# Kernel optimization log

Hardware: AMD Instinct MI355X
Metric: run time of the kernel (lower is better)

## Reference

```python
import jax, jax.numpy as jnp
import numpy as np
from jax import lax

DT = 0.01  # fixed Euler-Maruyama step size

B, N, C, M, H, T = 1024, 64, 16, 16, 512, 128


def setup_inputs() -> dict:
    key = jax.random.key(0)
    ks = jax.random.split(key, 8)
    d_in = N + C  # concat(y, control)
    inp = {
        "y0": jax.random.normal(ks[0], (B, N), jnp.float32),
        "controls": jax.random.normal(ks[1], (T, C), jnp.float32),
        "noise": jax.random.normal(ks[2], (T - 1, B, M), jnp.float32),
        # mu MLP: d_in -> H -> N
        "W1_mu": jax.random.normal(ks[3], (d_in, H), jnp.float32) / np.sqrt(d_in),
        "b1_mu": jnp.zeros((H,), jnp.float32),
        "W2_mu": jax.random.normal(ks[4], (H, N), jnp.float32) / np.sqrt(H),
        "b2_mu": jnp.zeros((N,), jnp.float32),
        # sigma MLP: d_in -> H -> N*M
        "W1_sg": jax.random.normal(ks[5], (d_in, H), jnp.float32) / np.sqrt(d_in),
        "b1_sg": jnp.zeros((H,), jnp.float32),
        "W2_sg": jax.random.normal(ks[6], (H, N * M), jnp.float32) / np.sqrt(H),
        "b2_sg": jnp.zeros((N * M,), jnp.float32),
    }
    return inp


def _mlp(x, W1, b1, W2, b2):
    return jnp.maximum(x @ W1 + b1, 0.0) @ W2 + b2


def reference(y0, controls, noise, W1_mu, b1_mu, W2_mu, b2_mu,
              W1_sg, b1_sg, W2_sg, b2_sg):
    """Euler-Maruyama solve of dy = f(y,u) dt + g(y,u) dW.
    Returns trajectory [T, B, N] including y0 (as torchsde.sdeint does)."""
    b, n = y0.shape
    m = noise.shape[-1]
    sqrt_dt = jnp.sqrt(jnp.asarray(DT, y0.dtype))

    def step(y, inp):
        u, z = inp  # u: [C] control at t_k, z: [B, M] standard normal
        x = jnp.concatenate([y, jnp.broadcast_to(u[None, :], (b, u.shape[0]))], axis=1)
        drift = _mlp(x, W1_mu, b1_mu, W2_mu, b2_mu)              # [B, N]
        diff = _mlp(x, W1_sg, b1_sg, W2_sg, b2_sg).reshape(b, n, m)  # [B, N, M]
        dW = z * sqrt_dt
        y_next = y + drift * DT + jnp.einsum('bnm,bm->bn', diff, dW)
        return y_next, y_next

    _, ys = lax.scan(step, y0, (controls[:-1], noise))
    return jnp.concatenate([y0[None], ys], axis=0)  # [T, B, N]
```

## Files before the change

### kernel.cpp

```cpp
#include <hip/hip_runtime.h>


typedef _Float16 f16x8 __attribute__((ext_vector_type(8)));
typedef float    f32x4 __attribute__((ext_vector_type(4)));

#define MFMA(a,b,c) __builtin_amdgcn_mfma_f32_16x16x32_f16(a,b,c,0,0,0)

#define Bb 1024
#define Tt 128
#define NG 64
#define GB 8
#define Rr 16
#define NT 512

#define W2SG_OFF 0
#define W2SG_HALVES (64*16*2*512)
#define W2MU_OFF (W2SG_OFF + W2SG_HALVES)
#define W2MU_HALVES (4*16*2*512)
#define W1MU_OFF (W2MU_OFF + W2MU_HALVES)
#define W1_HALVES (32*3*2*512)
#define W1SG_OFF (W1MU_OFF + W1_HALVES)
#define WS_HALVES (W1SG_OFF + W1_HALVES)
#define ACC_BYTES_OFF ((size_t)WS_HALVES * 2)
#define ACC_FLOATS (3 * NG * 1024)
#define CNT_BYTES_OFF (ACC_BYTES_OFF + (size_t)ACC_FLOATS * 4)
#define CNT_STRIDE 16

__global__ __launch_bounds__(256) void pack_weights(
    const float* __restrict__ W1_mu, const float* __restrict__ W2_mu,
    const float* __restrict__ W1_sg, const float* __restrict__ W2_sg,
    _Float16* __restrict__ wsh)
{
    int gid = blockIdx.x * 256 + threadIdx.x;
    if (gid >= 81920) return;
    const float* src; int ncols, kvalid; size_t dst;
    int id, tile, ks, lane;
    if (gid < 65536) {
        id = gid; tile = id >> 10; id &= 1023; ks = id >> 6; lane = id & 63;
        src = W2_sg; ncols = 1024; kvalid = 512;
        dst = W2SG_OFF + (size_t)((tile*16 + ks)*2) * 512 + lane*8;
    } else if (gid < 69632) {
        id = gid - 65536; tile = id >> 10; id &= 1023; ks = id >> 6; lane = id & 63;
        src = W2_mu; ncols = 64; kvalid = 512;
        dst = W2MU_OFF + (size_t)((tile*16 + ks)*2) * 512 + lane*8;
    } else if (gid < 75776) {
        id = gid - 69632; tile = id / 192; id %= 192; ks = id >> 6; lane = id & 63;
        src = W1_mu; ncols = 512; kvalid = 80;
        dst = W1MU_OFF + (size_t)((tile*3 + ks)*2) * 512 + lane*8;
    } else {
        id = gid - 75776; tile = id / 192; id %= 192; ks = id >> 6; lane = id & 63;
        src = W1_sg; ncols = 512; kvalid = 80;
        dst = W1SG_OFF + (size_t)((tile*3 + ks)*2) * 512 + lane*8;
    }
    const int n  = tile*16 + (lane & 15);
    const int kb = ks*32 + ((lane >> 4) << 3);
    f16x8 hi8, lo8;
    #pragma unroll
    for (int jj = 0; jj < 8; ++jj) {
        int k = kb + jj;
        float wv = (k < kvalid) ? src[(size_t)k * ncols + n] : 0.f;
        _Float16 h = (_Float16)wv;
        hi8[jj] = h;
        lo8[jj] = (_Float16)(wv - (float)h);
    }
    *((f16x8*)(wsh + dst))       = hi8;
    *((f16x8*)(wsh + dst + 512)) = lo8;
}

__global__ __launch_bounds__(NT, 4) void nsde_splitk(
    const float* __restrict__ y0, const float* __restrict__ controls,
    const float* __restrict__ noise,
    const float* __restrict__ b1_mu, const float* __restrict__ b2_mu,
    const float* __restrict__ b1_sg, const float* __restrict__ b2_sg,
    const _Float16* __restrict__ wf,
    float* __restrict__ accbuf, unsigned int* __restrict__ cnt,
    float* __restrict__ out)
{
    __shared__ _Float16 s_xhi[Rr][104], s_xlo[Rr][104];
    __shared__ _Float16 s_hhi[2][Rr][72], s_hlo[2][Rr][72];
    __shared__ float s_y[Rr*64];
    __shared__ float s_dw[Rr][16];
    __shared__ float s_part[Rr*64];
    __shared__ float s_pmu[Rr*64];

    const int tid  = threadIdx.x;
    const int lane = tid & 63, w = tid >> 6;
    const int m15  = lane & 15, quad = lane >> 4;
    const int j    = blockIdx.x & 7;
    const int g    = blockIdx.x >> 3;
    const int r0   = g * Rr;

    const int l  = w >> 2;
    const int ct = w & 3;
    const int tg = j*4 + ct;
    const _Float16* w1base = wf + (l ? W1SG_OFF : W1MU_OFF);
    const float bias1 = (l ? b1_sg : b1_mu)[j*64 + ct*16 + m15];
    float b2v[8];
    #pragma unroll
    for (int t = 0; t < 8; ++t)
        b2v[t] = (j == 0) ? b2_sg[(w + t*8)*16 + m15] : 0.f;
    const float b2m = (w < 4 && j == 0) ? b2_mu[w*16 + m15] * 0.01f : 0.f;

    for (int e = tid; e < Rr*24; e += NT) {
        int r = e / 24, c = 80 + e % 24;
        s_xhi[r][c] = (_Float16)0.f; s_xlo[r][c] = (_Float16)0.f;
    }
    if (tid < 256) {
        int e0 = tid*4, r = e0 >> 6, n = e0 & 63;
        float4 yv = *(const float4*)&y0[(size_t)(r0 + r)*64 + n];
        float vv[4] = {yv.x, yv.y, yv.z, yv.w};
        #pragma unroll
        for (int q = 0; q < 4; ++q) {
            s_y[e0+q] = vv[q];
            _Float16 h = (_Float16)vv[q];
            s_xhi[r][n+q] = h; s_xlo[r][n+q] = (_Float16)(vv[q] - (float)h);
        }
        if ((tid >> 5) == j)
            *(float4*)&out[(size_t)(r0 + r)*64 + n] = yv;
        int rr2 = tid >> 4, cc2 = tid & 15;
        float u = controls[cc2];
        _Float16 h = (_Float16)u;
        s_xhi[rr2][64+cc2] = h; s_xlo[rr2][64+cc2] = (_Float16)(u - (float)h);
        s_dw[rr2][cc2] = noise[(size_t)(r0 + rr2)*16 + cc2] * 0.1f;
    }
    __syncthreads();

    for (int k = 0; k < Tt-1; ++k) {
        {
            f32x4 a0 = {0,0,0,0}, a1 = {0,0,0,0}, a2 = {0,0,0,0};
            #pragma unroll
            for (int ks = 0; ks < 3; ++ks) {
                const _Float16* bp = w1base + (size_t)((tg*3 + ks)*2)*512 + lane*8;
                f16x8 bh = *(const f16x8*)bp;
                f16x8 bl = *(const f16x8*)(bp + 512);
                f16x8 ah = *(const f16x8*)&s_xhi[m15][ks*32 + quad*8];
                f16x8 al = *(const f16x8*)&s_xlo[m15][ks*32 + quad*8];
                a0 = MFMA(ah, bh, a0);
                a1 = MFMA(ah, bl, a1);
                a2 = MFMA(al, bh, a2);
            }
            f32x4 s = a0 + a1 + a2;
            #pragma unroll
            for (int rg = 0; rg < 4; ++rg) {
                int row = quad*4 + rg;
                float v = fmaxf(s[rg] + bias1, 0.f);
                _Float16 h = (_Float16)v;
                s_hhi[l][row][ct*16 + m15] = h;
                s_hlo[l][row][ct*16 + m15] = (_Float16)(v - (float)h);
            }
        }
        __syncthreads();

        float dwv[4];
        #pragma unroll
        for (int rg = 0; rg < 4; ++rg)
            dwv[rg] = s_dw[quad*4 + rg][m15];

        if (w < 4) {
            f16x8 Mh0 = *(const f16x8*)&s_hhi[0][m15][quad*8];
            f16x8 Ml0 = *(const f16x8*)&s_hlo[0][m15][quad*8];
            f16x8 Mh1 = *(const f16x8*)&s_hhi[0][m15][32 + quad*8];
            f16x8 Ml1 = *(const f16x8*)&s_hlo[0][m15][32 + quad*8];
            const _Float16* bp = wf + W2MU_OFF + (size_t)((w*16 + 2*j)*2)*512 + lane*8;
            f16x8 bh0 = *(const f16x8*)(bp);
            f16x8 bl0 = *(const f16x8*)(bp + 512);
            f16x8 bh1 = *(const f16x8*)(bp + 1024);
            f16x8 bl1 = *(const f16x8*)(bp + 1536);
            f32x4 hh = {0,0,0,0}, hl = {0,0,0,0}, lh = {0,0,0,0};
            hh = MFMA(Mh0, bh0, hh); hl = MFMA(Mh0, bl0, hl); lh = MFMA(Ml0, bh0, lh);
            hh = MFMA(Mh1, bh1, hh); hl = MFMA(Mh1, bl1, hl); lh = MFMA(Ml1, bh1, lh);
            f32x4 s = hh + hl + lh;
            #pragma unroll
            for (int rg = 0; rg < 4; ++rg)
                s_pmu[(quad*4 + rg)*64 + w*16 + m15] = s[rg]*0.01f + b2m;
        }

        f16x8 Ah0 = *(const f16x8*)&s_hhi[1][m15][quad*8];
        f16x8 Al0 = *(const f16x8*)&s_hlo[1][m15][quad*8];
        f16x8 Ah1 = *(const f16x8*)&s_hhi[1][m15][32 + quad*8];
        f16x8 Al1 = *(const f16x8*)&s_hlo[1][m15][32 + quad*8];
        #pragma unroll 2
        for (int t = 0; t < 8; ++t) {
            const int nt = w + t*8;
            const _Float16* bp = wf + W2SG_OFF + (size_t)((nt*16 + 2*j)*2)*512 + lane*8;
            f16x8 bh0 = *(const f16x8*)(bp);
            f16x8 bl0 = *(const f16x8*)(bp + 512);
            f16x8 bh1 = *(const f16x8*)(bp + 1024);
            f16x8 bl1 = *(const f16x8*)(bp + 1536);
            f32x4 hh = {0,0,0,0}, hl = {0,0,0,0}, lh = {0,0,0,0};
            hh = MFMA(Ah0, bh0, hh); hl = MFMA(Ah0, bl0, hl); lh = MFMA(Al0, bh0, lh);
            hh = MFMA(Ah1, bh1, hh); hl = MFMA(Ah1, bl1, hl); lh = MFMA(Al1, bh1, lh);
            f32x4 s = hh + hl + lh;
            #pragma unroll
            for (int rg = 0; rg < 4; ++rg) {
                float v = (s[rg] + b2v[t]) * dwv[rg];
                v += __shfl_xor(v, 1); v += __shfl_xor(v, 2);
                v += __shfl_xor(v, 4); v += __shfl_xor(v, 8);
                if (m15 == 0) s_part[(quad*4 + rg)*64 + nt] = v;
            }
        }
        __syncthreads();

        const int slot = k % 3;
        float* ab = accbuf + ((size_t)slot*NG + g)*1024;
        const int e0 = tid*2;
        {
            float v0 = s_part[e0]   + s_pmu[e0];
            float v1 = s_part[e0+1] + s_pmu[e0+1];
            __hip_atomic_fetch_add(&ab[e0],   v0, __ATOMIC_RELAXED,
                                   __HIP_MEMORY_SCOPE_AGENT);
            __hip_atomic_fetch_add(&ab[e0+1], v1, __ATOMIC_RELAXED,
                                   __HIP_MEMORY_SCOPE_AGENT);
        }
        __syncthreads();
        if (tid == 0) {
            __hip_atomic_fetch_add(&cnt[g*CNT_STRIDE], 1u, __ATOMIC_RELEASE,
                                   __HIP_MEMORY_SCOPE_AGENT);
            while (__hip_atomic_load(&cnt[g*CNT_STRIDE], __ATOMIC_RELAXED,
                                     __HIP_MEMORY_SCOPE_AGENT) < (unsigned)GB*(k+1))
                __builtin_amdgcn_s_sleep(2);
        }
        __syncthreads();

        {
            const int r = e0 >> 6, n = e0 & 63;
            float sum0 = __hip_atomic_load(&ab[e0], __ATOMIC_RELAXED,
                                           __HIP_MEMORY_SCOPE_AGENT);
            float sum1 = __hip_atomic_load(&ab[e0+1], __ATOMIC_RELAXED,
                                           __HIP_MEMORY_SCOPE_AGENT);
            float ya = s_y[e0]   + sum0;
            float yb = s_y[e0+1] + sum1;
            s_y[e0] = ya; s_y[e0+1] = yb;
            _Float16 ha = (_Float16)ya, hb = (_Float16)yb;
            s_xhi[r][n] = ha;   s_xlo[r][n]   = (_Float16)(ya - (float)ha);
            s_xhi[r][n+1] = hb; s_xlo[r][n+1] = (_Float16)(yb - (float)hb);
            if ((tid >> 6) == j) {
                float2 o = {ya, yb};
                *(float2*)&out[((size_t)(k+1)*Bb + r0 + r)*64 + n] = o;
                if (k >= 1) {
                    float* zb = accbuf + ((size_t)((k-1)%3)*NG + g)*1024;
                    __hip_atomic_store(&zb[e0],   0.f, __ATOMIC_RELAXED,
                                       __HIP_MEMORY_SCOPE_AGENT);
                    __hip_atomic_store(&zb[e0+1], 0.f, __ATOMIC_RELAXED,
                                       __HIP_MEMORY_SCOPE_AGENT);
                }
            }
        }
        if (k < Tt-2 && tid < 256) {
            int r = tid >> 4, c = tid & 15;
            float u = controls[(size_t)(k+1)*16 + c];
            _Float16 h = (_Float16)u;
            s_xhi[r][64+c] = h; s_xlo[r][64+c] = (_Float16)(u - (float)h);
            s_dw[r][c] = noise[((size_t)(k+1)*Bb + r0 + r)*16 + c] * 0.1f;
        }
        __syncthreads();
    }
}

extern "C" void kernel_launch(void* const* d_in, const int* in_sizes, int n_in,
                              void* d_out, int out_size, void* d_ws, size_t ws_size,
                              hipStream_t stream) {
    const float* y0       = (const float*)d_in[0];
    const float* controls = (const float*)d_in[1];
    const float* noise    = (const float*)d_in[2];
    const float* W1_mu    = (const float*)d_in[3];
    const float* b1_mu    = (const float*)d_in[4];
    const float* W2_mu    = (const float*)d_in[5];
    const float* b2_mu    = (const float*)d_in[6];
    const float* W1_sg    = (const float*)d_in[7];
    const float* b1_sg    = (const float*)d_in[8];
    const float* W2_sg    = (const float*)d_in[9];
    const float* b2_sg    = (const float*)d_in[10];
    float* out = (float*)d_out;
    _Float16* wsh = (_Float16*)d_ws;
    float* accbuf = (float*)((char*)d_ws + ACC_BYTES_OFF);
    unsigned int* cnt = (unsigned int*)((char*)d_ws + CNT_BYTES_OFF);

    hipMemsetAsync((char*)d_ws + ACC_BYTES_OFF, 0,
                   (size_t)ACC_FLOATS*4 + (size_t)NG*CNT_STRIDE*4, stream);
    pack_weights<<<320, 256, 0, stream>>>(W1_mu, W2_mu, W1_sg, W2_sg, wsh);
    nsde_splitk<<<NG*GB, NT, 0, stream>>>(y0, controls, noise,
                                          b1_mu, b2_mu, b1_sg, b2_sg,
                                          (const _Float16*)wsh,
                                          accbuf, cnt, out);
}
```

Before: 2.294 ms.

## Split hidden dimension across 16 blocks per row group instead of 8

Doubles the split-K factor so each block handles 32 hidden units instead of 64. Only four waves now compute the first layer, and the second-layer sigma tiles are spread unevenly, six per wave for waves 0-3 and ten per wave for waves 4-7, so the mu waves also take a share. The second-layer bias moves into shared memory and the occupancy hint rises to 8. The aim is more parallelism and occupancy across the device, at the cost of twice as many global atomic adds and barrier arrivals per step and idle waves during layer one.

New measurement: 4.000 ms. 74.4% more time.

```diff
diff --git a/kernel.cpp b/kernel.cpp
--- a/kernel.cpp
+++ b/kernel.cpp
@@ -9,7 +9,7 @@
 #define Bb 1024
 #define Tt 128
 #define NG 64
-#define GB 8
+#define GB 16
 #define Rr 16
 #define NT 512
 
@@ -67,7 +67,7 @@
     *((f16x8*)(wsh + dst + 512)) = lo8;
 }
 
-__global__ __launch_bounds__(NT, 4) void nsde_splitk(
+__global__ __launch_bounds__(NT, 8) void nsde_splitk(
     const float* __restrict__ y0, const float* __restrict__ controls,
     const float* __restrict__ noise,
     const float* __restrict__ b1_mu, const float* __restrict__ b2_mu,
@@ -77,34 +77,35 @@
     float* __restrict__ out)
 {
     __shared__ _Float16 s_xhi[Rr][104], s_xlo[Rr][104];
-    __shared__ _Float16 s_hhi[2][Rr][72], s_hlo[2][Rr][72];
+    __shared__ _Float16 s_hhi[2][Rr][36], s_hlo[2][Rr][36];
     __shared__ float s_y[Rr*64];
     __shared__ float s_dw[Rr][16];
     __shared__ float s_part[Rr*64];
     __shared__ float s_pmu[Rr*64];
+    __shared__ float s_b2sg[1024];
 
     const int tid  = threadIdx.x;
     const int lane = tid & 63, w = tid >> 6;
     const int m15  = lane & 15, quad = lane >> 4;
-    const int j    = blockIdx.x & 7;
-    const int g    = blockIdx.x >> 3;
+    const int j    = blockIdx.x & 15;
+    const int g    = blockIdx.x >> 4;
     const int r0   = g * Rr;
 
-    const int l  = w >> 2;
-    const int ct = w & 3;
-    const int tg = j*4 + ct;
+    const int l  = w >> 1;
+    const int ct = w & 1;
+    const int tg = j*2 + ct;
     const _Float16* w1base = wf + (l ? W1SG_OFF : W1MU_OFF);
-    const float bias1 = (l ? b1_sg : b1_mu)[j*64 + ct*16 + m15];
-    float b2v[8];
-    #pragma unroll
-    for (int t = 0; t < 8; ++t)
-        b2v[t] = (j == 0) ? b2_sg[(w + t*8)*16 + m15] : 0.f;
+    const float bias1 = (w < 4) ? (l ? b1_sg : b1_mu)[j*32 + ct*16 + m15] : 0.f;
     const float b2m = (w < 4 && j == 0) ? b2_mu[w*16 + m15] * 0.01f : 0.f;
+    const int ntile = (w < 4) ? 6 : 10;
+    const int nbase = (w < 4) ? w*6 : 24 + (w-4)*10;
 
     for (int e = tid; e < Rr*24; e += NT) {
         int r = e / 24, c = 80 + e % 24;
         s_xhi[r][c] = (_Float16)0.f; s_xlo[r][c] = (_Float16)0.f;
     }
+    for (int e = tid; e < 1024; e += NT)
+        s_b2sg[e] = (j == 0) ? b2_sg[e] : 0.f;
     if (tid < 256) {
         int e0 = tid*4, r = e0 >> 6, n = e0 & 63;
         float4 yv = *(const float4*)&y0[(size_t)(r0 + r)*64 + n];
@@ -115,7 +116,7 @@
             _Float16 h = (_Float16)vv[q];
             s_xhi[r][n+q] = h; s_xlo[r][n+q] = (_Float16)(vv[q] - (float)h);
         }
-        if ((tid >> 5) == j)
+        if ((tid >> 4) == j)
             *(float4*)&out[(size_t)(r0 + r)*64 + n] = yv;
         int rr2 = tid >> 4, cc2 = tid & 15;
         float u = controls[cc2];
@@ -126,7 +127,7 @@
     __syncthreads();
 
     for (int k = 0; k < Tt-1; ++k) {
-        {
+        if (w < 4) {
             f32x4 a0 = {0,0,0,0}, a1 = {0,0,0,0}, a2 = {0,0,0,0};
             #pragma unroll
             for (int ks = 0; ks < 3; ++ks) {
@@ -159,16 +160,11 @@
         if (w < 4) {
             f16x8 Mh0 = *(const f16x8*)&s_hhi[0][m15][quad*8];
             f16x8 Ml0 = *(const f16x8*)&s_hlo[0][m15][quad*8];
-            f16x8 Mh1 = *(const f16x8*)&s_hhi[0][m15][32 + quad*8];
-            f16x8 Ml1 = *(const f16x8*)&s_hlo[0][m15][32 + quad*8];
-            const _Float16* bp = wf + W2MU_OFF + (size_t)((w*16 + 2*j)*2)*512 + lane*8;
+            const _Float16* bp = wf + W2MU_OFF + (size_t)((w*16 + j)*2)*512 + lane*8;
             f16x8 bh0 = *(const f16x8*)(bp);
             f16x8 bl0 = *(const f16x8*)(bp + 512);
-            f16x8 bh1 = *(const f16x8*)(bp + 1024);
-            f16x8 bl1 = *(const f16x8*)(bp + 1536);
             f32x4 hh = {0,0,0,0}, hl = {0,0,0,0}, lh = {0,0,0,0};
             hh = MFMA(Mh0, bh0, hh); hl = MFMA(Mh0, bl0, hl); lh = MFMA(Ml0, bh0, lh);
-            hh = MFMA(Mh1, bh1, hh); hl = MFMA(Mh1, bl1, hl); lh = MFMA(Ml1, bh1, lh);
             f32x4 s = hh + hl + lh;
             #pragma unroll
             for (int rg = 0; rg < 4; ++rg)
@@ -177,23 +173,19 @@
 
         f16x8 Ah0 = *(const f16x8*)&s_hhi[1][m15][quad*8];
         f16x8 Al0 = *(const f16x8*)&s_hlo[1][m15][quad*8];
-        f16x8 Ah1 = *(const f16x8*)&s_hhi[1][m15][32 + quad*8];
-        f16x8 Al1 = *(const f16x8*)&s_hlo[1][m15][32 + quad*8];
         #pragma unroll 2
-        for (int t = 0; t < 8; ++t) {
-            const int nt = w + t*8;
-            const _Float16* bp = wf + W2SG_OFF + (size_t)((nt*16 + 2*j)*2)*512 + lane*8;
+        for (int t = 0; t < ntile; ++t) {
+            const int nt = nbase + t;
+            const _Float16* bp = wf + W2SG_OFF + (size_t)((nt*16 + j)*2)*512 + lane*8;
             f16x8 bh0 = *(const f16x8*)(bp);
             f16x8 bl0 = *(const f16x8*)(bp + 512);
-            f16x8 bh1 = *(const f16x8*)(bp + 1024);
-            f16x8 bl1 = *(const f16x8*)(bp + 1536);
             f32x4 hh = {0,0,0,0}, hl = {0,0,0,0}, lh = {0,0,0,0};
             hh = MFMA(Ah0, bh0, hh); hl = MFMA(Ah0, bl0, hl); lh = MFMA(Al0, bh0, lh);
-            hh = MFMA(Ah1, bh1, hh); hl = MFMA(Ah1, bl1, hl); lh = MFMA(Al1, bh1, lh);
             f32x4 s = hh + hl + lh;
+            const float b2v = s_b2sg[nt*16 + m15];
             #pragma unroll
             for (int rg = 0; rg < 4; ++rg) {
-                float v = (s[rg] + b2v[t]) * dwv[rg];
+                float v = (s[rg] + b2v) * dwv[rg];
                 v += __shfl_xor(v, 1); v += __shfl_xor(v, 2);
                 v += __shfl_xor(v, 4); v += __shfl_xor(v, 8);
                 if (m15 == 0) s_part[(quad*4 + rg)*64 + nt] = v;
@@ -234,7 +226,7 @@
             _Float16 ha = (_Float16)ya, hb = (_Float16)yb;
             s_xhi[r][n] = ha;   s_xlo[r][n]   = (_Float16)(ya - (float)ha);
             s_xhi[r][n+1] = hb; s_xlo[r][n+1] = (_Float16)(yb - (float)hb);
-            if ((tid >> 6) == j) {
+            if ((tid >> 5) == j) {
                 float2 o = {ya, yb};
                 *(float2*)&out[((size_t)(k+1)*Bb + r0 + r)*64 + n] = o;
                 if (k >= 1) {
```

## Replace split-K atomic reduction with output-column split and gather of partials

Applied to the files above, without the earlier changes.

Each of the 8 blocks per row group now computes the full hidden layer (all 512 sigma units and half of the mu units) redundantly, then owns a disjoint slice of the sigma output columns. Results go to double-buffered slots with plain atomic stores, and every block sums the three partial buffers after the counter barrier. This removes the float atomic adds, the zeroing of old accumulators and the host memset of the accumulators. In exchange each block does 8x more first-layer work and more second-layer K iterations, and launch bounds are raised to 6 waves/SIMD, which may constrain registers.

Measured after the change: 3.307 ms. 44.2% more time.

```diff
diff --git a/kernel.cpp b/kernel.cpp
--- a/kernel.cpp
+++ b/kernel.cpp
@@ -21,9 +21,11 @@
 #define W1_HALVES (32*3*2*512)
 #define W1SG_OFF (W1MU_OFF + W1_HALVES)
 #define WS_HALVES (W1SG_OFF + W1_HALVES)
-#define ACC_BYTES_OFF ((size_t)WS_HALVES * 2)
-#define ACC_FLOATS (3 * NG * 1024)
-#define CNT_BYTES_OFF (ACC_BYTES_OFF + (size_t)ACC_FLOATS * 4)
+
+#define PSG_OFF  ((size_t)WS_HALVES * 2)
+#define PMUA_OFF (PSG_OFF  + (size_t)2*NG*1024*4)
+#define PMUB_OFF (PMUA_OFF + (size_t)2*NG*1024*4)
+#define CNT_OFF  (PMUB_OFF + (size_t)2*NG*1024*4)
 #define CNT_STRIDE 16
 
 __global__ __launch_bounds__(256) void pack_weights(
@@ -67,21 +69,21 @@
     *((f16x8*)(wsh + dst + 512)) = lo8;
 }
 
-__global__ __launch_bounds__(NT, 4) void nsde_splitk(
+__global__ __launch_bounds__(NT, 6) void nsde_gather(
     const float* __restrict__ y0, const float* __restrict__ controls,
     const float* __restrict__ noise,
     const float* __restrict__ b1_mu, const float* __restrict__ b2_mu,
     const float* __restrict__ b1_sg, const float* __restrict__ b2_sg,
     const _Float16* __restrict__ wf,
-    float* __restrict__ accbuf, unsigned int* __restrict__ cnt,
+    float* __restrict__ psg, float* __restrict__ pmua,
+    float* __restrict__ pmub, unsigned int* __restrict__ cnt,
     float* __restrict__ out)
 {
     __shared__ _Float16 s_xhi[Rr][104], s_xlo[Rr][104];
-    __shared__ _Float16 s_hhi[2][Rr][72], s_hlo[2][Rr][72];
+    __shared__ _Float16 s_sghi[Rr][520], s_sglo[Rr][520];
+    __shared__ _Float16 s_muhi[Rr][264], s_mulo[Rr][264];
     __shared__ float s_y[Rr*64];
     __shared__ float s_dw[Rr][16];
-    __shared__ float s_part[Rr*64];
-    __shared__ float s_pmu[Rr*64];
 
     const int tid  = threadIdx.x;
     const int lane = tid & 63, w = tid >> 6;
@@ -89,17 +91,17 @@
     const int j    = blockIdx.x & 7;
     const int g    = blockIdx.x >> 3;
     const int r0   = g * Rr;
-
-    const int l  = w >> 2;
-    const int ct = w & 3;
-    const int tg = j*4 + ct;
-    const _Float16* w1base = wf + (l ? W1SG_OFF : W1MU_OFF);
-    const float bias1 = (l ? b1_sg : b1_mu)[j*64 + ct*16 + m15];
-    float b2v[8];
+    const int muhh = (j >= 4);
+
+    float b1sgv[4], b1muv[2];
     #pragma unroll
-    for (int t = 0; t < 8; ++t)
-        b2v[t] = (j == 0) ? b2_sg[(w + t*8)*16 + m15] : 0.f;
-    const float b2m = (w < 4 && j == 0) ? b2_mu[w*16 + m15] * 0.01f : 0.f;
+    for (int i = 0; i < 4; ++i) b1sgv[i] = b1_sg[(w*4+i)*16 + m15];
+    #pragma unroll
+    for (int i = 0; i < 2; ++i) b1muv[i] = b1_mu[(w*2+i + muhh*16)*16 + m15];
+    const int nsg = j*8 + w;
+    const float b2sgv = b2_sg[nsg*16 + m15];
+    const int tm = j & 3;
+    const float b2muv = (j < 4) ? b2_mu[tm*16 + m15]*0.01f : 0.f;
 
     for (int e = tid; e < Rr*24; e += NT) {
         int r = e / 24, c = 80 + e % 24;
@@ -126,93 +128,117 @@
     __syncthreads();
 
     for (int k = 0; k < Tt-1; ++k) {
-        {
+        f16x8 xah[3], xal[3];
+        #pragma unroll
+        for (int ks = 0; ks < 3; ++ks) {
+            xah[ks] = *(const f16x8*)&s_xhi[m15][ks*32 + quad*8];
+            xal[ks] = *(const f16x8*)&s_xlo[m15][ks*32 + quad*8];
+        }
+        #pragma unroll 2
+        for (int i = 0; i < 4; ++i) {
+            const int t = w*4 + i;
             f32x4 a0 = {0,0,0,0}, a1 = {0,0,0,0}, a2 = {0,0,0,0};
             #pragma unroll
             for (int ks = 0; ks < 3; ++ks) {
-                const _Float16* bp = w1base + (size_t)((tg*3 + ks)*2)*512 + lane*8;
+                const _Float16* bp = wf + W1SG_OFF + (size_t)((t*3+ks)*2)*512 + lane*8;
                 f16x8 bh = *(const f16x8*)bp;
                 f16x8 bl = *(const f16x8*)(bp + 512);
-                f16x8 ah = *(const f16x8*)&s_xhi[m15][ks*32 + quad*8];
-                f16x8 al = *(const f16x8*)&s_xlo[m15][ks*32 + quad*8];
-                a0 = MFMA(ah, bh, a0);
-                a1 = MFMA(ah, bl, a1);
-                a2 = MFMA(al, bh, a2);
+                a0 = MFMA(xah[ks], bh, a0);
+                a1 = MFMA(xah[ks], bl, a1);
+                a2 = MFMA(xal[ks], bh, a2);
             }
             f32x4 s = a0 + a1 + a2;
             #pragma unroll
             for (int rg = 0; rg < 4; ++rg) {
                 int row = quad*4 + rg;
-                float v = fmaxf(s[rg] + bias1, 0.f);
+                float v = fmaxf(s[rg] + b1sgv[i], 0.f);
                 _Float16 h = (_Float16)v;
-                s_hhi[l][row][ct*16 + m15] = h;
-                s_hlo[l][row][ct*16 + m15] = (_Float16)(v - (float)h);
+                s_sghi[row][t*16+m15] = h;
+                s_sglo[row][t*16+m15] = (_Float16)(v - (float)h);
+            }
+        }
+        #pragma unroll
+        for (int i = 0; i < 2; ++i) {
+            const int tl = w*2 + i;
+            const int tgm = tl + muhh*16;
+            f32x4 a0 = {0,0,0,0}, a1 = {0,0,0,0}, a2 = {0,0,0,0};
+            #pragma unroll
+            for (int ks = 0; ks < 3; ++ks) {
+                const _Float16* bp = wf + W1MU_OFF + (size_t)((tgm*3+ks)*2)*512 + lane*8;
+                f16x8 bh = *(const f16x8*)bp;
+                f16x8 bl = *(const f16x8*)(bp + 512);
+                a0 = MFMA(xah[ks], bh, a0);
+                a1 = MFMA(xah[ks], bl, a1);
+                a2 = MFMA(xal[ks], bh, a2);
+            }
+            f32x4 s = a0 + a1 + a2;
+            #pragma unroll
+            for (int rg = 0; rg < 4; ++rg) {
+                int row = quad*4 + rg;
+                float v = fmaxf(s[rg] + b1muv[i], 0.f);
+                _Float16 h = (_Float16)v;
+                s_muhi[row][tl*16+m15] = h;
+                s_mulo[row][tl*16+m15] = (_Float16)(v - (float)h);
             }
         }
         __syncthreads();
+
+        const int slot = k & 1;
+        float* psg_s  = psg  + ((size_t)slot*NG + g)*1024;
+        float* pmua_s = pmua + ((size_t)slot*NG + g)*1024;
+        float* pmub_s = pmub + ((size_t)slot*NG + g)*1024;
 
         float dwv[4];
         #pragma unroll
         for (int rg = 0; rg < 4; ++rg)
             dwv[rg] = s_dw[quad*4 + rg][m15];
 
-        if (w < 4) {
-            f16x8 Mh0 = *(const f16x8*)&s_hhi[0][m15][quad*8];
-            f16x8 Ml0 = *(const f16x8*)&s_hlo[0][m15][quad*8];
-            f16x8 Mh1 = *(const f16x8*)&s_hhi[0][m15][32 + quad*8];
-            f16x8 Ml1 = *(const f16x8*)&s_hlo[0][m15][32 + quad*8];
-            const _Float16* bp = wf + W2MU_OFF + (size_t)((w*16 + 2*j)*2)*512 + lane*8;
-            f16x8 bh0 = *(const f16x8*)(bp);
-            f16x8 bl0 = *(const f16x8*)(bp + 512);
-            f16x8 bh1 = *(const f16x8*)(bp + 1024);
-            f16x8 bl1 = *(const f16x8*)(bp + 1536);
+        {
             f32x4 hh = {0,0,0,0}, hl = {0,0,0,0}, lh = {0,0,0,0};
-            hh = MFMA(Mh0, bh0, hh); hl = MFMA(Mh0, bl0, hl); lh = MFMA(Ml0, bh0, lh);
-            hh = MFMA(Mh1, bh1, hh); hl = MFMA(Mh1, bl1, hl); lh = MFMA(Ml1, bh1, lh);
+            #pragma unroll 2
+            for (int ks = 0; ks < 16; ++ks) {
+                const _Float16* bp = wf + W2SG_OFF + (size_t)((nsg*16+ks)*2)*512 + lane*8;
+                f16x8 bh = *(const f16x8*)bp;
+                f16x8 bl = *(const f16x8*)(bp + 512);
+                f16x8 ah = *(const f16x8*)&s_sghi[m15][ks*32 + quad*8];
+                f16x8 al = *(const f16x8*)&s_sglo[m15][ks*32 + quad*8];
+                hh = MFMA(ah, bh, hh); hl = MFMA(ah, bl, hl); lh = MFMA(al, bh, lh);
+            }
             f32x4 s = hh + hl + lh;
             #pragma unroll
-            for (int rg = 0; rg < 4; ++rg)
-                s_pmu[(quad*4 + rg)*64 + w*16 + m15] = s[rg]*0.01f + b2m;
-        }
-
-        f16x8 Ah0 = *(const f16x8*)&s_hhi[1][m15][quad*8];
-        f16x8 Al0 = *(const f16x8*)&s_hlo[1][m15][quad*8];
-        f16x8 Ah1 = *(const f16x8*)&s_hhi[1][m15][32 + quad*8];
-        f16x8 Al1 = *(const f16x8*)&s_hlo[1][m15][32 + quad*8];
-        #pragma unroll 2
-        for (int t = 0; t < 8; ++t) {
-            const int nt = w + t*8;
-            const _Float16* bp = wf + W2SG_OFF + (size_t)((nt*16 + 2*j)*2)*512 + lane*8;
-            f16x8 bh0 = *(const f16x8*)(bp);
-            f16x8 bl0 = *(const f16x8*)(bp + 512);
-            f16x8 bh1 = *(const f16x8*)(bp + 1024);
-            f16x8 bl1 = *(const f16x8*)(bp + 1536);
-            f32x4 hh = {0,0,0,0}, hl = {0,0,0,0}, lh = {0,0,0,0};
-            hh = MFMA(Ah0, bh0, hh); hl = MFMA(Ah0, bl0, hl); lh = MFMA(Al0, bh0, lh);
-            hh = MFMA(Ah1, bh1, hh); hl = MFMA(Ah1, bl1, hl); lh = MFMA(Al1, bh1, lh);
-            f32x4 s = hh + hl + lh;
-            #pragma unroll
             for (int rg = 0; rg < 4; ++rg) {
-                float v = (s[rg] + b2v[t]) * dwv[rg];
+                float v = (s[rg] + b2sgv) * dwv[rg];
                 v += __shfl_xor(v, 1); v += __shfl_xor(v, 2);
                 v += __shfl_xor(v, 4); v += __shfl_xor(v, 8);
-                if (m15 == 0) s_part[(quad*4 + rg)*64 + nt] = v;
+                if (m15 == 0)
+                    __hip_atomic_store(&psg_s[(quad*4+rg)*64 + nsg], v,
+                                       __ATOMIC_RELAXED, __HIP_MEMORY_SCOPE_AGENT);
+            }
+        }
+
+        if (w == 7) {
+            f32x4 hh = {0,0,0,0}, hl = {0,0,0,0}, lh = {0,0,0,0};
+            #pragma unroll 2
+            for (int ksl = 0; ksl < 8; ++ksl) {
+                const int ks = ksl + muhh*8;
+                const _Float16* bp = wf + W2MU_OFF + (size_t)((tm*16+ks)*2)*512 + lane*8;
+                f16x8 bh = *(const f16x8*)bp;
+                f16x8 bl = *(const f16x8*)(bp + 512);
+                f16x8 ah = *(const f16x8*)&s_muhi[m15][ksl*32 + quad*8];
+                f16x8 al = *(const f16x8*)&s_mulo[m15][ksl*32 + quad*8];
+                hh = MFMA(ah, bh, hh); hl = MFMA(ah, bl, hl); lh = MFMA(al, bh, lh);
+            }
+            f32x4 s = hh + hl + lh;
+            float* pd = (j < 4) ? pmua_s : pmub_s;
+            #pragma unroll
+            for (int rg = 0; rg < 4; ++rg) {
+                float v = s[rg]*0.01f + b2muv;
+                __hip_atomic_store(&pd[(quad*4+rg)*64 + tm*16 + m15], v,
+                                   __ATOMIC_RELAXED, __HIP_MEMORY_SCOPE_AGENT);
             }
         }
         __syncthreads();
 
-        const int slot = k % 3;
-        float* ab = accbuf + ((size_t)slot*NG + g)*1024;
-        const int e0 = tid*2;
-        {
-            float v0 = s_part[e0]   + s_pmu[e0];
-            float v1 = s_part[e0+1] + s_pmu[e0+1];
-            __hip_atomic_fetch_add(&ab[e0],   v0, __ATOMIC_RELAXED,
-                                   __HIP_MEMORY_SCOPE_AGENT);
-            __hip_atomic_fetch_add(&ab[e0+1], v1, __ATOMIC_RELAXED,
-                                   __HIP_MEMORY_SCOPE_AGENT);
-        }
-        __syncthreads();
         if (tid == 0) {
             __hip_atomic_fetch_add(&cnt[g*CNT_STRIDE], 1u, __ATOMIC_RELEASE,
                                    __HIP_MEMORY_SCOPE_AGENT);
@@ -223,27 +249,26 @@
         __syncthreads();
 
         {
+            const int e0 = tid*2;
             const int r = e0 >> 6, n = e0 & 63;
-            float sum0 = __hip_atomic_load(&ab[e0], __ATOMIC_RELAXED,
-                                           __HIP_MEMORY_SCOPE_AGENT);
-            float sum1 = __hip_atomic_load(&ab[e0+1], __ATOMIC_RELAXED,
-                                           __HIP_MEMORY_SCOPE_AGENT);
-            float ya = s_y[e0]   + sum0;
-            float yb = s_y[e0+1] + sum1;
-            s_y[e0] = ya; s_y[e0+1] = yb;
-            _Float16 ha = (_Float16)ya, hb = (_Float16)yb;
-            s_xhi[r][n] = ha;   s_xlo[r][n]   = (_Float16)(ya - (float)ha);
-            s_xhi[r][n+1] = hb; s_xlo[r][n+1] = (_Float16)(yb - (float)hb);
+            float yv[2];
+            #pragma unroll
+            for (int q = 0; q < 2; ++q) {
+                const int e = e0 + q;
+                float sum = __hip_atomic_load(&psg_s[e], __ATOMIC_RELAXED,
+                                              __HIP_MEMORY_SCOPE_AGENT)
+                          + __hip_atomic_load(&pmua_s[e], __ATOMIC_RELAXED,
+                                              __HIP_MEMORY_SCOPE_AGENT)
+                          + __hip_atomic_load(&pmub_s[e], __ATOMIC_RELAXED,
+                                              __HIP_MEMORY_SCOPE_AGENT);
+                float y = s_y[e] + sum;
+                s_y[e] = y; yv[q] = y;
+                _Float16 h = (_Float16)y;
+                s_xhi[r][n+q] = h; s_xlo[r][n+q] = (_Float16)(y - (float)h);
+            }
             if ((tid >> 6) == j) {
-                float2 o = {ya, yb};
+                float2 o = {yv[0], yv[1]};
                 *(float2*)&out[((size_t)(k+1)*Bb + r0 + r)*64 + n] = o;
-                if (k >= 1) {
-                    float* zb = accbuf + ((size_t)((k-1)%3)*NG + g)*1024;
-                    __hip_atomic_store(&zb[e0],   0.f, __ATOMIC_RELAXED,
-                                       __HIP_MEMORY_SCOPE_AGENT);
-                    __hip_atomic_store(&zb[e0+1], 0.f, __ATOMIC_RELAXED,
-                                       __HIP_MEMORY_SCOPE_AGENT);
-                }
             }
         }
         if (k < Tt-2 && tid < 256) {
@@ -273,14 +298,15 @@
     const float* b2_sg    = (const float*)d_in[10];
     float* out = (float*)d_out;
     _Float16* wsh = (_Float16*)d_ws;
-    float* accbuf = (float*)((char*)d_ws + ACC_BYTES_OFF);
-    unsigned int* cnt = (unsigned int*)((char*)d_ws + CNT_BYTES_OFF);
-
-    hipMemsetAsync((char*)d_ws + ACC_BYTES_OFF, 0,
-                   (size_t)ACC_FLOATS*4 + (size_t)NG*CNT_STRIDE*4, stream);
+    float* psg  = (float*)((char*)d_ws + PSG_OFF);
+    float* pmua = (float*)((char*)d_ws + PMUA_OFF);
+    float* pmub = (float*)((char*)d_ws + PMUB_OFF);
+    unsigned int* cnt = (unsigned int*)((char*)d_ws + CNT_OFF);
+
+    hipMemsetAsync((char*)d_ws + CNT_OFF, 0, (size_t)NG*CNT_STRIDE*4, stream);
     pack_weights<<<320, 256, 0, stream>>>(W1_mu, W2_mu, W1_sg, W2_sg, wsh);
-    nsde_splitk<<<NG*GB, NT, 0, stream>>>(y0, controls, noise,
+    nsde_gather<<<NG*GB, NT, 0, stream>>>(y0, controls, noise,
                                           b1_mu, b2_mu, b1_sg, b2_sg,
                                           (const _Float16*)wsh,
-                                          accbuf, cnt, out);
+                                          psg, pmua, pmub, cnt, out);
 }
```
